# Performance work log

Hardware: AMD Instinct MI355X
Metric: run time of the kernel (lower is better)

The kernel has to match this reference:

```python
import jax, jax.numpy as jnp
import numpy as np
from jax import lax

B, N, C, H, W = 8, 256, 512, 8, 8
DIM = C * 2  # 1024
HW = H * W


def setup_inputs() -> dict:
    key = jax.random.key(0)
    ks = jax.random.split(key, 8)
    x = jax.random.normal(ks[0], (B, N, C, H, W), dtype=jnp.float32)
    # 3 frozen conv1d(1,1,k=5) layers: kaiming-normal weights, zero bias
    conv_w = jax.random.normal(ks[1], (3, 5), dtype=jnp.float32) * np.float32(np.sqrt(2.0 / 5.0))
    conv_b = jnp.zeros((3,), dtype=jnp.float32)
    # 512 tiny Linear(HW, 2): weight [out,in] stacked -> [C, 2, HW], trunc-normal std=0.01
    Ws = (jax.random.truncated_normal(ks[2], -2.0, 2.0, (C, 2, HW), dtype=jnp.float32) * 0.01)
    bs = jnp.zeros((C, 2), dtype=jnp.float32)
    # frozen fc Linear(DIM, DIM)
    fc_w = (jax.random.truncated_normal(ks[3], -2.0, 2.0, (DIM, DIM), dtype=jnp.float32) * 0.01)
    fc_b = jnp.zeros((DIM,), dtype=jnp.float32)
    return {"x": x, "conv_w": conv_w, "conv_b": conv_b, "Ws": Ws, "bs": bs, "fc_w": fc_w, "fc_b": fc_b}


def _conv1d_same(a, w, b):
    # a: [B, N], w: [5], b: scalar; cross-correlation with padding 2 (same as torch Conv1d)
    out = lax.conv_general_dilated(a[:, None, :], w[None, None, :], (1,), [(2, 2)])
    return out[:, 0, :] + b


def reference(x, conv_w, conv_b, Ws, bs, fc_w, fc_b):
    # Channel (patch) attention loop, 3 iterations
    for i in range(3):
        att = x.mean(axis=(2, 3, 4))                      # AdaptiveAvgPool1d(1) over (C H W) -> [B, N]
        att = jax.nn.sigmoid(_conv1d_same(att, conv_w[i], conv_b[i]))  # [B, N]
        x = x * att[:, :, None, None, None]
    xf = x.reshape(B, N, C, HW)
    # 512 per-channel Linear(HW, 2) as one grouped contraction
    y = jnp.einsum('bnch,coh->bnco', xf, Ws) + bs          # [B, N, C, 2]
    y = y.reshape(B, N, C * 2)                             # [B, N, 1024]
    out = y @ fc_w.T + fc_b                                # frozen fc
    # dropout in eval mode = identity
    return out
```

## Files before the change

### kernel.cpp

```cpp
#include <hip/hip_runtime.h>
#include <hip/hip_bf16.h>


typedef unsigned short u16;
typedef unsigned int u32;
typedef __attribute__((ext_vector_type(8))) short short8;
typedef __attribute__((ext_vector_type(4))) float floatx4;

#define Bb 8
#define Nn 256
#define Cc 512
#define HWs 64
#define BN 2048
#define DIMd 1024

__device__ inline u16 f2bf(float f) {
    unsigned int u = __builtin_bit_cast(unsigned int, f);
    unsigned int r = (u + 0x7FFFu + ((u >> 16) & 1u)) >> 16;
    return (u16)r;
}

__global__ __launch_bounds__(256) void k0a_cvt_w(
    const float* __restrict__ w, u16* __restrict__ wb)
{
    const int i = blockIdx.x * 256 + threadIdx.x;
    floatx4 v = ((const floatx4*)w)[i];
    u32 lo = (u32)f2bf(v[0]) | ((u32)f2bf(v[1]) << 16);
    u32 hi = (u32)f2bf(v[2]) | ((u32)f2bf(v[3]) << 16);
    ((u32*)wb)[i * 2 + 0] = lo;
    ((u32*)wb)[i * 2 + 1] = hi;
}

__global__ __launch_bounds__(256) void k0b_bias(
    const float* __restrict__ bs, const float* __restrict__ fc_w,
    const float* __restrict__ fc_b, float* __restrict__ bias2)
{
    const int wv = blockIdx.x * 4 + (threadIdx.x >> 6);
    const int lane = threadIdx.x & 63;
    const floatx4* bp = (const floatx4*)(fc_w + (size_t)wv * DIMd + lane * 16);
    const floatx4* sp = (const floatx4*)(bs + lane * 16);
    float s = 0.f;
    #pragma unroll
    for (int v = 0; v < 4; ++v) {
        floatx4 a = bp[v], b = sp[v];
        #pragma unroll
        for (int j = 0; j < 4; ++j) s += a[j] * b[j];
    }
    #pragma unroll
    for (int sft = 32; sft; sft >>= 1) s += __shfl_xor(s, sft);
    if (lane == 0) bias2[wv] = s + fc_b[wv];
}

__global__ __launch_bounds__(256) void k1_reduce_grouped(
    const float* __restrict__ x, const float* __restrict__ Ws,
    u16* __restrict__ ybf, float* __restrict__ m0)
{
    const int bid = blockIdx.x;
    const int tid = threadIdx.x;
    const float* xb = x + (size_t)bid * (Cc * HWs);
    const int q = tid & 3;
    const int cofs = tid >> 2;
    float lsum = 0.f;

    for (int p = 0; p < 8; ++p) {
        const int c = p * 64 + cofs;
        const floatx4* xp  = (const floatx4*)(xb + p * 4096 + tid * 16);
        const floatx4* w0p = (const floatx4*)(Ws + (size_t)(c * 2 + 0) * HWs + q * 16);
        const floatx4* w1p = (const floatx4*)(Ws + (size_t)(c * 2 + 1) * HWs + q * 16);
        float d0 = 0.f, d1 = 0.f;
        #pragma unroll
        for (int v = 0; v < 4; ++v) {
            floatx4 xv = xp[v];
            floatx4 w0 = w0p[v];
            floatx4 w1 = w1p[v];
            #pragma unroll
            for (int j = 0; j < 4; ++j) {
                d0 += xv[j] * w0[j];
                d1 += xv[j] * w1[j];
                lsum += xv[j];
            }
        }
        d0 += __shfl_xor(d0, 1); d0 += __shfl_xor(d0, 2);
        d1 += __shfl_xor(d1, 1); d1 += __shfl_xor(d1, 2);
        if (q == 0) {
            u32 pk = (u32)f2bf(d0) | ((u32)f2bf(d1) << 16);
            ((u32*)ybf)[(size_t)bid * (DIMd / 2) + c] = pk;
        }
    }
    #pragma unroll
    for (int s = 32; s; s >>= 1) lsum += __shfl_xor(lsum, s);
    __shared__ float wsum[4];
    if ((tid & 63) == 0) wsum[tid >> 6] = lsum;
    __syncthreads();
    if (tid == 0)
        m0[bid] = (wsum[0] + wsum[1] + wsum[2] + wsum[3]) * (1.0f / 32768.f);
}

__global__ __launch_bounds__(256) void k2_scale(
    const float* __restrict__ m0, const float* __restrict__ conv_w,
    const float* __restrict__ conv_b, float* __restrict__ scale)
{
    const int b = blockIdx.x;
    const int n = threadIdx.x;
    __shared__ float buf[Nn];
    float a = m0[b * Nn + n];
    float p = 1.f;
    for (int i = 0; i < 3; ++i) {
        buf[n] = a;
        __syncthreads();
        float t = 0.f;
        #pragma unroll
        for (int k = 0; k < 5; ++k) {
            int idx = n + k - 2;
            float v = (idx >= 0 && idx < Nn) ? buf[idx] : 0.f;
            t += v * conv_w[i * 5 + k];
        }
        t += conv_b[i];
        float s = 1.f / (1.f + __expf(-t));
        p *= s;
        a *= s;
        __syncthreads();
    }
    scale[b * Nn + n] = p;
}

__global__ __launch_bounds__(256) void k3_gemm(
    const u16* __restrict__ ybf, const u16* __restrict__ wbf,
    const float* __restrict__ scale, const float* __restrict__ bias2,
    float* __restrict__ out)
{
    const int tid = threadIdx.x;
    const int w = tid >> 6;
    const int lane = tid & 63;
    const int l15 = lane & 15;
    const int quad = lane >> 4;
    const int wm = w & 1, wn = w >> 1;
    const int r0 = blockIdx.x * 64 + wm * 32;
    const int c0 = blockIdx.y * 64 + wn * 32;

    floatx4 acc[2][2] = {};
    const u16* aptr0 = ybf + (size_t)(r0 + l15) * DIMd + quad * 8;
    const u16* aptr1 = aptr0 + 16 * DIMd;
    const u16* bptr0 = wbf + (size_t)(c0 + l15) * DIMd + quad * 8;
    const u16* bptr1 = bptr0 + 16 * DIMd;

    for (int k0 = 0; k0 < DIMd; k0 += 32) {
        short8 a0 = *(const short8*)(aptr0 + k0);
        short8 a1 = *(const short8*)(aptr1 + k0);
        short8 b0 = *(const short8*)(bptr0 + k0);
        short8 b1 = *(const short8*)(bptr1 + k0);
        acc[0][0] = __builtin_amdgcn_mfma_f32_16x16x32_bf16(a0, b0, acc[0][0], 0, 0, 0);
        acc[0][1] = __builtin_amdgcn_mfma_f32_16x16x32_bf16(a0, b1, acc[0][1], 0, 0, 0);
        acc[1][0] = __builtin_amdgcn_mfma_f32_16x16x32_bf16(a1, b0, acc[1][0], 0, 0, 0);
        acc[1][1] = __builtin_amdgcn_mfma_f32_16x16x32_bf16(a1, b1, acc[1][1], 0, 0, 0);
    }

    #pragma unroll
    for (int ni = 0; ni < 2; ++ni) {
        const int col = c0 + ni * 16 + l15;
        const float b2 = bias2[col];
        #pragma unroll
        for (int mi = 0; mi < 2; ++mi) {
            #pragma unroll
            for (int r = 0; r < 4; ++r) {
                const int row = r0 + mi * 16 + quad * 4 + r;
                out[(size_t)row * DIMd + col] = scale[row] * acc[mi][ni][r] + b2;
            }
        }
    }
}

extern "C" void kernel_launch(void* const* d_in, const int* in_sizes, int n_in,
                              void* d_out, int out_size, void* d_ws, size_t ws_size,
                              hipStream_t stream) {
    const float* x      = (const float*)d_in[0];
    const float* conv_w = (const float*)d_in[1];
    const float* conv_b = (const float*)d_in[2];
    const float* Ws     = (const float*)d_in[3];
    const float* bs     = (const float*)d_in[4];
    const float* fc_w   = (const float*)d_in[5];
    const float* fc_b   = (const float*)d_in[6];
    float* out = (float*)d_out;

    float* m0    = (float*)d_ws;
    float* scale = m0 + BN;
    float* bias2 = scale + BN;
    u16*   ybf   = (u16*)(bias2 + DIMd);
    u16*   wbf   = ybf + (size_t)BN * DIMd;

    k0a_cvt_w<<<dim3(1024), dim3(256), 0, stream>>>(fc_w, wbf);
    k0b_bias<<<dim3(256), dim3(256), 0, stream>>>(bs, fc_w, fc_b, bias2);
    k1_reduce_grouped<<<dim3(BN), dim3(256), 0, stream>>>(x, Ws, ybf, m0);
    k2_scale<<<dim3(Bb), dim3(Nn), 0, stream>>>(m0, conv_w, conv_b, scale);
    k3_gemm<<<dim3(32, 16), dim3(256), 0, stream>>>(ybf, wbf, scale, bias2, out);
}
```

Baseline: 423.4 us.

## Merge prep kernels into one launch, nontemporal x loads, unroll GEMM k-loop

Measured after the change: 443.0 us. +4.6%, slower.

```diff
diff --git a/kernel.cpp b/kernel.cpp
--- a/kernel.cpp
+++ b/kernel.cpp
@@ -20,37 +20,6 @@
     return (u16)r;
 }
 
-__global__ __launch_bounds__(256) void k0a_cvt_w(
-    const float* __restrict__ w, u16* __restrict__ wb)
-{
-    const int i = blockIdx.x * 256 + threadIdx.x;
-    floatx4 v = ((const floatx4*)w)[i];
-    u32 lo = (u32)f2bf(v[0]) | ((u32)f2bf(v[1]) << 16);
-    u32 hi = (u32)f2bf(v[2]) | ((u32)f2bf(v[3]) << 16);
-    ((u32*)wb)[i * 2 + 0] = lo;
-    ((u32*)wb)[i * 2 + 1] = hi;
-}
-
-__global__ __launch_bounds__(256) void k0b_bias(
-    const float* __restrict__ bs, const float* __restrict__ fc_w,
-    const float* __restrict__ fc_b, float* __restrict__ bias2)
-{
-    const int wv = blockIdx.x * 4 + (threadIdx.x >> 6);
-    const int lane = threadIdx.x & 63;
-    const floatx4* bp = (const floatx4*)(fc_w + (size_t)wv * DIMd + lane * 16);
-    const floatx4* sp = (const floatx4*)(bs + lane * 16);
-    float s = 0.f;
-    #pragma unroll
-    for (int v = 0; v < 4; ++v) {
-        floatx4 a = bp[v], b = sp[v];
-        #pragma unroll
-        for (int j = 0; j < 4; ++j) s += a[j] * b[j];
-    }
-    #pragma unroll
-    for (int sft = 32; sft; sft >>= 1) s += __shfl_xor(s, sft);
-    if (lane == 0) bias2[wv] = s + fc_b[wv];
-}
-
 __global__ __launch_bounds__(256) void k1_reduce_grouped(
     const float* __restrict__ x, const float* __restrict__ Ws,
     u16* __restrict__ ybf, float* __restrict__ m0)
@@ -70,7 +39,7 @@
         float d0 = 0.f, d1 = 0.f;
         #pragma unroll
         for (int v = 0; v < 4; ++v) {
-            floatx4 xv = xp[v];
+            floatx4 xv = __builtin_nontemporal_load(xp + v);
             floatx4 w0 = w0p[v];
             floatx4 w1 = w1p[v];
             #pragma unroll
@@ -96,32 +65,60 @@
         m0[bid] = (wsum[0] + wsum[1] + wsum[2] + wsum[3]) * (1.0f / 32768.f);
 }
 
-__global__ __launch_bounds__(256) void k2_scale(
+__global__ __launch_bounds__(256) void k2_misc(
+    const float* __restrict__ fc_w, u16* __restrict__ wbf,
+    const float* __restrict__ bs, const float* __restrict__ fc_b,
+    float* __restrict__ bias2,
     const float* __restrict__ m0, const float* __restrict__ conv_w,
     const float* __restrict__ conv_b, float* __restrict__ scale)
 {
-    const int b = blockIdx.x;
-    const int n = threadIdx.x;
-    __shared__ float buf[Nn];
-    float a = m0[b * Nn + n];
-    float p = 1.f;
-    for (int i = 0; i < 3; ++i) {
-        buf[n] = a;
-        __syncthreads();
-        float t = 0.f;
+    const int bid = blockIdx.x;
+    if (bid < 1024) {
+        const int i = bid * 256 + threadIdx.x;
+        floatx4 v = ((const floatx4*)fc_w)[i];
+        u32 lo = (u32)f2bf(v[0]) | ((u32)f2bf(v[1]) << 16);
+        u32 hi = (u32)f2bf(v[2]) | ((u32)f2bf(v[3]) << 16);
+        ((u32*)wbf)[i * 2 + 0] = lo;
+        ((u32*)wbf)[i * 2 + 1] = hi;
+    } else if (bid < 1280) {
+        const int wv = (bid - 1024) * 4 + (threadIdx.x >> 6);
+        const int lane = threadIdx.x & 63;
+        const floatx4* bp = (const floatx4*)(fc_w + (size_t)wv * DIMd + lane * 16);
+        const floatx4* sp = (const floatx4*)(bs + lane * 16);
+        float s = 0.f;
         #pragma unroll
-        for (int k = 0; k < 5; ++k) {
-            int idx = n + k - 2;
-            float v = (idx >= 0 && idx < Nn) ? buf[idx] : 0.f;
-            t += v * conv_w[i * 5 + k];
+        for (int v = 0; v < 4; ++v) {
+            floatx4 a = bp[v], b = sp[v];
+            #pragma unroll
+            for (int j = 0; j < 4; ++j) s += a[j] * b[j];
         }
-        t += conv_b[i];
-        float s = 1.f / (1.f + __expf(-t));
-        p *= s;
-        a *= s;
-        __syncthreads();
+        #pragma unroll
+        for (int sft = 32; sft; sft >>= 1) s += __shfl_xor(s, sft);
+        if (lane == 0) bias2[wv] = s + fc_b[wv];
+    } else {
+        const int b = bid - 1280;
+        const int n = threadIdx.x;
+        __shared__ float buf[Nn];
+        float a = m0[b * Nn + n];
+        float p = 1.f;
+        for (int i = 0; i < 3; ++i) {
+            buf[n] = a;
+            __syncthreads();
+            float t = 0.f;
+            #pragma unroll
+            for (int k = 0; k < 5; ++k) {
+                int idx = n + k - 2;
+                float v = (idx >= 0 && idx < Nn) ? buf[idx] : 0.f;
+                t += v * conv_w[i * 5 + k];
+            }
+            t += conv_b[i];
+            float s = 1.f / (1.f + __expf(-t));
+            p *= s;
+            a *= s;
+            __syncthreads();
+        }
+        scale[b * Nn + n] = p;
     }
-    scale[b * Nn + n] = p;
 }
 
 __global__ __launch_bounds__(256) void k3_gemm(
@@ -144,6 +141,7 @@
     const u16* bptr0 = wbf + (size_t)(c0 + l15) * DIMd + quad * 8;
     const u16* bptr1 = bptr0 + 16 * DIMd;
 
+    #pragma unroll 4
     for (int k0 = 0; k0 < DIMd; k0 += 32) {
         short8 a0 = *(const short8*)(aptr0 + k0);
         short8 a1 = *(const short8*)(aptr1 + k0);
@@ -188,9 +186,8 @@
     u16*   ybf   = (u16*)(bias2 + DIMd);
     u16*   wbf   = ybf + (size_t)BN * DIMd;
 
-    k0a_cvt_w<<<dim3(1024), dim3(256), 0, stream>>>(fc_w, wbf);
-    k0b_bias<<<dim3(256), dim3(256), 0, stream>>>(bs, fc_w, fc_b, bias2);
     k1_reduce_grouped<<<dim3(BN), dim3(256), 0, stream>>>(x, Ws, ybf, m0);
-    k2_scale<<<dim3(Bb), dim3(Nn), 0, stream>>>(m0, conv_w, conv_b, scale);
+    k2_misc<<<dim3(1288), dim3(256), 0, stream>>>(fc_w, wbf, bs, fc_b, bias2,
+                                                  m0, conv_w, conv_b, scale);
     k3_gemm<<<dim3(32, 16), dim3(256), 0, stream>>>(ybf, wbf, scale, bias2, out);
 }
```
